# Kernel optimization log

Measured on AMD Instinct MI355X. Metric: run time of the kernel, lower is better.

## Reference

```python
import jax, jax.numpy as jnp
import numpy as np

DIM = 256
H = 4
D = DIM // H  # head_dim = 64
SCALE = D ** -0.5


def setup_inputs() -> dict:
    key = jax.random.key(0)
    ks = jax.random.split(key, 12)
    B, N, M = 4, 2048, 2048
    x_query = jax.random.normal(ks[0], (B, N, DIM), dtype=jnp.float32)
    x_context = jax.random.normal(ks[1], (B, M, DIM), dtype=jnp.float32)
    geo_bias = jax.random.normal(ks[2], (B, H, N, M), dtype=jnp.float32)
    init = 1.0 / np.sqrt(DIM)
    Wq = jax.random.uniform(ks[3], (DIM, DIM), jnp.float32, -init, init)
    bq = jax.random.uniform(ks[4], (DIM,), jnp.float32, -init, init)
    Wk = jax.random.uniform(ks[5], (DIM, DIM), jnp.float32, -init, init)
    bk = jax.random.uniform(ks[6], (DIM,), jnp.float32, -init, init)
    Wv = jax.random.uniform(ks[7], (DIM, DIM), jnp.float32, -init, init)
    bv = jax.random.uniform(ks[8], (DIM,), jnp.float32, -init, init)
    Wo = jax.random.uniform(ks[9], (DIM, DIM), jnp.float32, -init, init)
    bo = jax.random.uniform(ks[10], (DIM,), jnp.float32, -init, init)
    return {"x_query": x_query, "x_context": x_context, "geo_bias": geo_bias,
            "Wq": Wq, "bq": bq, "Wk": Wk, "bk": bk, "Wv": Wv, "bv": bv,
            "Wo": Wo, "bo": bo}


def reference(x_query, x_context, geo_bias, Wq, bq, Wk, bk, Wv, bv, Wo, bo):
    B, N, _ = x_query.shape
    M = x_context.shape[1]
    # projections; nn.Linear computes x @ W.T + b
    q = (x_query @ Wq.T + bq).reshape(B, N, H, D).transpose(0, 2, 1, 3)   # (B,H,N,D)
    k = (x_context @ Wk.T + bk).reshape(B, M, H, D).transpose(0, 2, 1, 3)  # (B,H,M,D)
    v = (x_context @ Wv.T + bv).reshape(B, M, H, D).transpose(0, 2, 1, 3)  # (B,H,M,D)
    attn = jnp.einsum("bhnd,bhmd->bhnm", q, k) * SCALE + geo_bias
    attn = jax.nn.softmax(attn, axis=-1)
    out = jnp.einsum("bhnm,bhmd->bhnd", attn, v)
    out = out.transpose(0, 2, 1, 3).reshape(B, N, DIM)
    return out @ Wo.T + bo
```

## Files before the change

### kernel.cpp

```cpp
#include <hip/hip_runtime.h>

typedef unsigned short u16;
typedef unsigned int u32;
using bf16x8  = __attribute__((ext_vector_type(8))) __bf16;
using u16x8   = __attribute__((ext_vector_type(8), may_alias)) u16;
using u16x4   = __attribute__((ext_vector_type(4), may_alias)) u16;
using f32x4   = __attribute__((ext_vector_type(4))) float;
using f32x4_a = __attribute__((ext_vector_type(4), may_alias)) float;

#define DEV __device__ __forceinline__

constexpr int Bn = 4, Hn = 4, Nn = 2048, Mn = 2048, Dn = 64, DIMn = 256;
constexpr float SCALEc = 0.125f;
constexpr float SHIFTc = 12.0f;
constexpr int LSTRIDE = 152;

DEV float bf2f(u16 h) { u32 u = ((u32)h) << 16; return __builtin_bit_cast(float, u); }
DEV u16 f2bf(float f) {
    u32 u = __builtin_bit_cast(u32, f);
    u += 0x7fffu + ((u >> 16) & 1u);
    return (u16)(u >> 16);
}
DEV bf16x8 ld8bf(const u16* p) {
    return __builtin_bit_cast(bf16x8, *reinterpret_cast<const u16x8*>(p));
}
DEV bf16x8 ld8f_bf(const float* p) {
    const f32x4 a = *reinterpret_cast<const f32x4_a*>(p);
    const f32x4 b = *reinterpret_cast<const f32x4_a*>(p + 4);
    u16x8 r;
    r[0] = f2bf(a[0]); r[1] = f2bf(a[1]); r[2] = f2bf(a[2]); r[3] = f2bf(a[3]);
    r[4] = f2bf(b[0]); r[5] = f2bf(b[1]); r[6] = f2bf(b[2]); r[7] = f2bf(b[3]);
    return __builtin_bit_cast(bf16x8, r);
}

typedef __attribute__((address_space(1))) const unsigned int as1_uint;
typedef __attribute__((address_space(3))) unsigned int as3_uint;
DEV void dma16(const float* g, float* l) {
    __builtin_amdgcn_global_load_lds((as1_uint*)g, (as3_uint*)l, 16, 0, 0);
}

__global__ __launch_bounds__(256) void qkv_kernel(
    const float* __restrict__ Xq, const float* __restrict__ Wq, const float* __restrict__ bq,
    const float* __restrict__ Xc, const float* __restrict__ Wk, const float* __restrict__ bk,
    const float* __restrict__ Wv, const float* __restrict__ bv,
    float* __restrict__ Q, u16* __restrict__ K, u16* __restrict__ V)
{
    const int wave = threadIdx.x >> 6, lane = threadIdx.x & 63;
    const int quad = lane >> 4, l16 = lane & 15;
    const int o0 = wave * 64;

    if (blockIdx.x < 512) {
        const int row0 = blockIdx.x * 16;
        const int b = row0 >> 11, n0 = row0 & 2047;
        f32x4 acc[4] = {};
        #pragma unroll
        for (int k0 = 0; k0 < 256; k0 += 32) {
            const bf16x8 af = ld8f_bf(Xq + (size_t)(row0 + l16) * DIMn + k0 + quad * 8);
            #pragma unroll
            for (int os = 0; os < 4; os++) {
                const bf16x8 wf = ld8f_bf(Wq + (size_t)(o0 + os * 16 + l16) * DIMn + k0 + quad * 8);
                acc[os] = __builtin_amdgcn_mfma_f32_16x16x32_bf16(af, wf, acc[os], 0, 0, 0);
            }
        }
        #pragma unroll
        for (int os = 0; os < 4; os++) {
            const int col = o0 + os * 16 + l16;
            const int h = col >> 6, d = col & 63;
            const float bb = bq[col];
            #pragma unroll
            for (int r = 0; r < 4; r++) {
                const int n = n0 + quad * 4 + r;
                Q[((size_t)(b * Hn + h) * Nn + n) * Dn + d] = acc[os][r] + bb;
            }
        }
    } else {
        const int row0 = (blockIdx.x - 512) * 16;
        const int b = row0 >> 11, n0 = row0 & 2047;
        f32x4 ack[4] = {};
        f32x4 acv[4] = {};
        #pragma unroll
        for (int k0 = 0; k0 < 256; k0 += 32) {
            const bf16x8 af = ld8f_bf(Xc + (size_t)(row0 + l16) * DIMn + k0 + quad * 8);
            #pragma unroll
            for (int os = 0; os < 4; os++) {
                const bf16x8 wkf = ld8f_bf(Wk + (size_t)(o0 + os * 16 + l16) * DIMn + k0 + quad * 8);
                ack[os] = __builtin_amdgcn_mfma_f32_16x16x32_bf16(af, wkf, ack[os], 0, 0, 0);
                const bf16x8 wvf = ld8f_bf(Wv + (size_t)(o0 + os * 16 + l16) * DIMn + k0 + quad * 8);
                acv[os] = __builtin_amdgcn_mfma_f32_16x16x32_bf16(wvf, af, acv[os], 0, 0, 0);
            }
        }
        #pragma unroll
        for (int os = 0; os < 4; os++) {
            const int col = o0 + os * 16 + l16;
            const int h = col >> 6, d = col & 63;
            const float bb = bk[col];
            #pragma unroll
            for (int r = 0; r < 4; r++) {
                const int m = n0 + quad * 4 + r;
                K[((size_t)(b * Hn + h) * Mn + m) * Dn + d] = f2bf(ack[os][r] + bb);
            }
        }
        #pragma unroll
        for (int os = 0; os < 4; os++)
            #pragma unroll
            for (int r = 0; r < 4; r++) {
                const int colf = o0 + os * 16 + quad * 4 + r;
                const int h = colf >> 6, d = colf & 63;
                const float bb = bv[colf];
                const int m = n0 + l16;
                V[((size_t)(b * Hn + h) * Dn + d) * Mn + m] = f2bf(acv[os][r] + bb);
            }
    }
}

__global__ __launch_bounds__(256) void attn_kernel(
    const float* __restrict__ Q,
    const u16* __restrict__ K,
    const u16* __restrict__ V,
    const float* __restrict__ geo,
    float* __restrict__ Pnum,
    float* __restrict__ Lsum,
    int S)
{
    __shared__ __align__(16) u16 plds[4][16 * LSTRIDE];
    __shared__ __align__(16) float glds[4][8][256];

    const int h = blockIdx.y;
    const int b = blockIdx.z / S, split = blockIdx.z % S;
    const int wave = threadIdx.x >> 6, lane = threadIdx.x & 63;
    const int quad = lane >> 4, l16 = lane & 15;
    const int nbase = blockIdx.x * 64 + wave * 16;
    const int mlen = Mn / S, mbeg = split * mlen, mend = mbeg + mlen;

    const float* Qh = Q + ((size_t)(b * Hn + h) * Nn + nbase) * Dn;
    const u16*   Kh = K + (size_t)(b * Hn + h) * Mn * Dn;
    const u16*   Vh = V + (size_t)(b * Hn + h) * Dn * Mn;
    const float* Gl = geo + ((size_t)(b * Hn + h) * Nn + nbase + l16) * (size_t)Mn + quad * 4;

    bf16x8 qh[2], ql[2];
    #pragma unroll
    for (int kh = 0; kh < 2; kh++) {
        const float* qp = Qh + (size_t)l16 * Dn + kh * 32 + quad * 8;
        const f32x4 a = *reinterpret_cast<const f32x4_a*>(qp);
        const f32x4 c = *reinterpret_cast<const f32x4_a*>(qp + 4);
        u16x8 hi, lo;
        #pragma unroll
        for (int j = 0; j < 4; j++) {
            hi[j] = f2bf(a[j]); lo[j] = f2bf(a[j] - bf2f(hi[j]));
            hi[4 + j] = f2bf(c[j]); lo[4 + j] = f2bf(c[j] - bf2f(hi[4 + j]));
        }
        qh[kh] = __builtin_bit_cast(bf16x8, hi);
        ql[kh] = __builtin_bit_cast(bf16x8, lo);
    }

    f32x4 oacc[4] = {};
    float lsum = 0.f;
    u16* pl = &plds[wave][0];
    float* gw = &glds[wave][0][0];
    const float* gr = gw + lane * 4;
    const u16* kbase = Kh + (size_t)l16 * Dn + quad * 8;
    const u16* vbase = Vh + (size_t)l16 * Mn + quad * 8;

    #pragma unroll
    for (int ms = 0; ms < 8; ms++)
        dma16(Gl + mbeg + ms * 16, gw + ms * 256);
    bf16x8 kb0 = ld8bf(kbase + (size_t)mbeg * Dn);
    bf16x8 kb1 = ld8bf(kbase + (size_t)mbeg * Dn + 32);

    for (int m0 = mbeg; m0 < mend; m0 += 128) {
        asm volatile("s_waitcnt vmcnt(0)" ::: "memory");
        #pragma unroll
        for (int ms = 0; ms < 8; ms++) {
            int mb = m0 + (ms + 1) * 16;
            if (mb > mend - 16) mb = mend - 16;
            const u16* kp = kbase + (size_t)mb * Dn;
            const bf16x8 nk0 = ld8bf(kp);
            const bf16x8 nk1 = ld8bf(kp + 32);
            f32x4 s = {};
            __builtin_amdgcn_s_setprio(1);
            s = __builtin_amdgcn_mfma_f32_16x16x32_bf16(kb0, qh[0], s, 0, 0, 0);
            s = __builtin_amdgcn_mfma_f32_16x16x32_bf16(kb0, ql[0], s, 0, 0, 0);
            s = __builtin_amdgcn_mfma_f32_16x16x32_bf16(kb1, qh[1], s, 0, 0, 0);
            s = __builtin_amdgcn_mfma_f32_16x16x32_bf16(kb1, ql[1], s, 0, 0, 0);
            __builtin_amdgcn_s_setprio(0);
            const f32x4 g = *reinterpret_cast<const f32x4_a*>(gr + ms * 256);
            u16x4 pk;
            float ls = 0.f;
            #pragma unroll
            for (int r = 0; r < 4; r++) {
                const float p = __expf(fmaf(s[r], SCALEc, g[r]) - SHIFTc);
                ls += p;
                pk[r] = f2bf(p);
            }
            lsum += ls;
            *reinterpret_cast<u16x4*>(pl + l16 * LSTRIDE + ms * 16 + quad * 4) = pk;
            kb0 = nk0; kb1 = nk1;
        }
        if (m0 + 128 < mend) {
            asm volatile("s_waitcnt lgkmcnt(0)" ::: "memory");
            #pragma unroll
            for (int ms = 0; ms < 8; ms++)
                dma16(Gl + (m0 + 128) + ms * 16, gw + ms * 256);
        }
        bf16x8 vcur[4], vnxt[4];
        #pragma unroll
        for (int ds = 0; ds < 4; ds++)
            vcur[ds] = ld8bf(vbase + (size_t)(ds * 16) * Mn + m0);
        #pragma unroll
        for (int kh = 0; kh < 4; kh++) {
            if (kh < 3) {
                #pragma unroll
                for (int ds = 0; ds < 4; ds++)
                    vnxt[ds] = ld8bf(vbase + (size_t)(ds * 16) * Mn + m0 + (kh + 1) * 32);
            }
            const bf16x8 pa = ld8bf(pl + l16 * LSTRIDE + kh * 32 + quad * 8);
            __builtin_amdgcn_s_setprio(1);
            #pragma unroll
            for (int ds = 0; ds < 4; ds++)
                oacc[ds] = __builtin_amdgcn_mfma_f32_16x16x32_bf16(pa, vcur[ds], oacc[ds], 0, 0, 0);
            __builtin_amdgcn_s_setprio(0);
            #pragma unroll
            for (int ds = 0; ds < 4; ds++) vcur[ds] = vnxt[ds];
        }
    }

    lsum += __shfl_xor(lsum, 16);
    lsum += __shfl_xor(lsum, 32);

    float* PN = Pnum + (size_t)split * (Bn * (size_t)Nn * DIMn)
                     + ((size_t)b * Nn + nbase) * DIMn + h * Dn;
    #pragma unroll
    for (int r = 0; r < 4; r++)
        #pragma unroll
        for (int ds = 0; ds < 4; ds++)
            PN[(size_t)(quad * 4 + r) * DIMn + ds * 16 + l16] = oacc[ds][r];

    if (lane < 16)
        Lsum[(((size_t)split * Bn + b) * Hn + h) * Nn + nbase + l16] = lsum;
}

__global__ __launch_bounds__(256) void oproj_kernel(
    const float* __restrict__ Pnum, const float* __restrict__ Lsum,
    const float* __restrict__ W, const float* __restrict__ bias,
    float* __restrict__ out, int S)
{
    const int row0 = blockIdx.x * 16;
    const int wave = threadIdx.x >> 6, lane = threadIdx.x & 63;
    const int quad = lane >> 4, l16 = lane & 15;
    const int o0 = wave * 64;
    const size_t slab = (size_t)Bn * Nn * DIMn;

    const int arow = row0 + l16;
    const int b = arow >> 11, n = arow & 2047;
    float inv[4];
    #pragma unroll
    for (int hh = 0; hh < 4; hh++) {
        float l = 0.f;
        for (int s = 0; s < S; s++)
            l += Lsum[(((size_t)s * Bn + b) * Hn + hh) * Nn + n];
        inv[hh] = 1.0f / l;
    }

    f32x4 acc[4] = {};
    #pragma unroll
    for (int k0 = 0; k0 < 256; k0 += 32) {
        f32x4 a0 = {}, a1 = {};
        for (int s = 0; s < S; s++) {
            const float* p = Pnum + (size_t)s * slab + (size_t)arow * DIMn + k0 + quad * 8;
            a0 += *reinterpret_cast<const f32x4_a*>(p);
            a1 += *reinterpret_cast<const f32x4_a*>(p + 4);
        }
        const float iv = inv[(k0 + quad * 8) >> 6];
        u16x8 r;
        #pragma unroll
        for (int j = 0; j < 4; j++) {
            r[j]     = f2bf(a0[j] * iv);
            r[4 + j] = f2bf(a1[j] * iv);
        }
        const bf16x8 af = __builtin_bit_cast(bf16x8, r);
        #pragma unroll
        for (int os = 0; os < 4; os++) {
            const bf16x8 wf = ld8f_bf(W + (size_t)(o0 + os * 16 + l16) * DIMn + k0 + quad * 8);
            acc[os] = __builtin_amdgcn_mfma_f32_16x16x32_bf16(af, wf, acc[os], 0, 0, 0);
        }
    }
    #pragma unroll
    for (int os = 0; os < 4; os++) {
        const int col = o0 + os * 16 + l16;
        const float bb = bias[col];
        #pragma unroll
        for (int r = 0; r < 4; r++) {
            const int row = row0 + quad * 4 + r;
            out[(size_t)row * DIMn + col] = acc[os][r] + bb;
        }
    }
}

extern "C" void kernel_launch(void* const* d_in, const int* in_sizes, int n_in,
                              void* d_out, int out_size, void* d_ws, size_t ws_size,
                              hipStream_t stream) {
    const float* xq  = (const float*)d_in[0];
    const float* xc  = (const float*)d_in[1];
    const float* geo = (const float*)d_in[2];
    const float* Wq  = (const float*)d_in[3];
    const float* bq  = (const float*)d_in[4];
    const float* Wk  = (const float*)d_in[5];
    const float* bk  = (const float*)d_in[6];
    const float* Wv  = (const float*)d_in[7];
    const float* bv  = (const float*)d_in[8];
    const float* Wo  = (const float*)d_in[9];
    const float* bo  = (const float*)d_in[10];

    const int S = (ws_size >= (60ull << 20)) ? 4 : 1;

    char* ws = (char*)d_ws;
    float* Qw   = (float*)ws;
    u16*   Kw   = (u16*)(ws + (8ull << 20));
    u16*   Vw   = (u16*)(ws + (12ull << 20));
    float* Pnum = (float*)(ws + (20ull << 20));
    float* Lsum = (float*)(ws + (20ull << 20) + (size_t)S * (8ull << 20));

    qkv_kernel<<<1024, 256, 0, stream>>>(xq, Wq, bq, xc, Wk, bk, Wv, bv, Qw, Kw, Vw);
    attn_kernel<<<dim3(Nn / 64, Hn, Bn * S), 256, 0, stream>>>(Qw, Kw, Vw, geo, Pnum, Lsum, S);
    oproj_kernel<<<Bn * Nn / 16, 256, 0, stream>>>(Pnum, Lsum, Wo, bo, (float*)d_out, S);
}
```

Before: 553.8 us.

## Use single-wave attention blocks with double-buffered 64-column geo bias tiles

The attention kernel becomes one wave per block, with 16 query rows each and 4x more blocks. It now steps over 64 context columns at a time, using a two-slot LDS ring for geo-bias DMA and a partial vmcnt wait so the next tile can stream in during compute. The PV step loads V directly per 32-wide chunk instead of software-prefetching it, and the split-M factor drops from 4 to 2. This trades intra-block wave sharing for a smaller LDS footprint and finer-grained overlap, but it risks less V latency hiding and correctness issues from the new wait count and buffer indexing.

```diff
diff --git a/kernel.cpp b/kernel.cpp
--- a/kernel.cpp
+++ b/kernel.cpp
@@ -13,7 +13,7 @@
 constexpr int Bn = 4, Hn = 4, Nn = 2048, Mn = 2048, Dn = 64, DIMn = 256;
 constexpr float SCALEc = 0.125f;
 constexpr float SHIFTc = 12.0f;
-constexpr int LSTRIDE = 152;
+constexpr int LSTRIDE = 76;
 
 DEV float bf2f(u16 h) { u32 u = ((u32)h) << 16; return __builtin_bit_cast(float, u); }
 DEV u16 f2bf(float f) {
@@ -113,7 +113,7 @@
     }
 }
 
-__global__ __launch_bounds__(256) void attn_kernel(
+__global__ __launch_bounds__(64) void attn_kernel(
     const float* __restrict__ Q,
     const u16* __restrict__ K,
     const u16* __restrict__ V,
@@ -122,14 +122,14 @@
     float* __restrict__ Lsum,
     int S)
 {
-    __shared__ __align__(16) u16 plds[4][16 * LSTRIDE];
-    __shared__ __align__(16) float glds[4][8][256];
+    __shared__ __align__(16) u16 plds[16 * LSTRIDE];
+    __shared__ __align__(16) float glds[2][4][256];
 
     const int h = blockIdx.y;
     const int b = blockIdx.z / S, split = blockIdx.z % S;
-    const int wave = threadIdx.x >> 6, lane = threadIdx.x & 63;
+    const int lane = threadIdx.x & 63;
     const int quad = lane >> 4, l16 = lane & 15;
-    const int nbase = blockIdx.x * 64 + wave * 16;
+    const int nbase = blockIdx.x * 16;
     const int mlen = Mn / S, mbeg = split * mlen, mend = mbeg + mlen;
 
     const float* Qh = Q + ((size_t)(b * Hn + h) * Nn + nbase) * Dn;
@@ -155,22 +155,24 @@
 
     f32x4 oacc[4] = {};
     float lsum = 0.f;
-    u16* pl = &plds[wave][0];
-    float* gw = &glds[wave][0][0];
-    const float* gr = gw + lane * 4;
     const u16* kbase = Kh + (size_t)l16 * Dn + quad * 8;
     const u16* vbase = Vh + (size_t)l16 * Mn + quad * 8;
 
     #pragma unroll
-    for (int ms = 0; ms < 8; ms++)
-        dma16(Gl + mbeg + ms * 16, gw + ms * 256);
+    for (int ms = 0; ms < 4; ms++)
+        dma16(Gl + mbeg + ms * 16, &glds[0][ms][0]);
+    #pragma unroll
+    for (int ms = 0; ms < 4; ms++)
+        dma16(Gl + mbeg + 64 + ms * 16, &glds[1][ms][0]);
     bf16x8 kb0 = ld8bf(kbase + (size_t)mbeg * Dn);
     bf16x8 kb1 = ld8bf(kbase + (size_t)mbeg * Dn + 32);
 
-    for (int m0 = mbeg; m0 < mend; m0 += 128) {
-        asm volatile("s_waitcnt vmcnt(0)" ::: "memory");
-        #pragma unroll
-        for (int ms = 0; ms < 8; ms++) {
+    int buf = 0;
+    for (int m0 = mbeg; m0 < mend; m0 += 64, buf ^= 1) {
+        asm volatile("s_waitcnt vmcnt(6)" ::: "memory");
+        const float* gr = &glds[buf][0][0] + lane * 4;
+        #pragma unroll
+        for (int ms = 0; ms < 4; ms++) {
             int mb = m0 + (ms + 1) * 16;
             if (mb > mend - 16) mb = mend - 16;
             const u16* kp = kbase + (size_t)mb * Dn;
@@ -193,34 +195,27 @@
                 pk[r] = f2bf(p);
             }
             lsum += ls;
-            *reinterpret_cast<u16x4*>(pl + l16 * LSTRIDE + ms * 16 + quad * 4) = pk;
+            *reinterpret_cast<u16x4*>(plds + l16 * LSTRIDE + ms * 16 + quad * 4) = pk;
             kb0 = nk0; kb1 = nk1;
+        }
+        #pragma unroll
+        for (int kh = 0; kh < 2; kh++) {
+            const bf16x8 pa = ld8bf(plds + l16 * LSTRIDE + kh * 32 + quad * 8);
+            bf16x8 vb[4];
+            #pragma unroll
+            for (int ds = 0; ds < 4; ds++)
+                vb[ds] = ld8bf(vbase + (size_t)(ds * 16) * Mn + m0 + kh * 32);
+            __builtin_amdgcn_s_setprio(1);
+            #pragma unroll
+            for (int ds = 0; ds < 4; ds++)
+                oacc[ds] = __builtin_amdgcn_mfma_f32_16x16x32_bf16(pa, vb[ds], oacc[ds], 0, 0, 0);
+            __builtin_amdgcn_s_setprio(0);
         }
         if (m0 + 128 < mend) {
             asm volatile("s_waitcnt lgkmcnt(0)" ::: "memory");
             #pragma unroll
-            for (int ms = 0; ms < 8; ms++)
-                dma16(Gl + (m0 + 128) + ms * 16, gw + ms * 256);
-        }
-        bf16x8 vcur[4], vnxt[4];
-        #pragma unroll
-        for (int ds = 0; ds < 4; ds++)
-            vcur[ds] = ld8bf(vbase + (size_t)(ds * 16) * Mn + m0);
-        #pragma unroll
-        for (int kh = 0; kh < 4; kh++) {
-            if (kh < 3) {
-                #pragma unroll
-                for (int ds = 0; ds < 4; ds++)
-                    vnxt[ds] = ld8bf(vbase + (size_t)(ds * 16) * Mn + m0 + (kh + 1) * 32);
-            }
-            const bf16x8 pa = ld8bf(pl + l16 * LSTRIDE + kh * 32 + quad * 8);
-            __builtin_amdgcn_s_setprio(1);
-            #pragma unroll
-            for (int ds = 0; ds < 4; ds++)
-                oacc[ds] = __builtin_amdgcn_mfma_f32_16x16x32_bf16(pa, vcur[ds], oacc[ds], 0, 0, 0);
-            __builtin_amdgcn_s_setprio(0);
-            #pragma unroll
-            for (int ds = 0; ds < 4; ds++) vcur[ds] = vnxt[ds];
+            for (int ms = 0; ms < 4; ms++)
+                dma16(Gl + (m0 + 128) + ms * 16, &glds[buf][ms][0]);
         }
     }
 
@@ -311,7 +306,7 @@
     const float* Wo  = (const float*)d_in[9];
     const float* bo  = (const float*)d_in[10];
 
-    const int S = (ws_size >= (60ull << 20)) ? 4 : 1;
+    const int S = (ws_size >= (40ull << 20)) ? 2 : 1;
 
     char* ws = (char*)d_ws;
     float* Qw   = (float*)ws;
@@ -321,6 +316,6 @@
     float* Lsum = (float*)(ws + (20ull << 20) + (size_t)S * (8ull << 20));
 
     qkv_kernel<<<1024, 256, 0, stream>>>(xq, Wq, bq, xc, Wk, bk, Wv, bv, Qw, Kw, Vw);
-    attn_kernel<<<dim3(Nn / 64, Hn, Bn * S), 256, 0, stream>>>(Qw, Kw, Vw, geo, Pnum, Lsum, S);
+    attn_kernel<<<dim3(Nn / 16, Hn, Bn * S), 64, 0, stream>>>(Qw, Kw, Vw, geo, Pnum, Lsum, S);
     oproj_kernel<<<Bn * Nn / 16, 256, 0, stream>>>(Pnum, Lsum, Wo, bo, (float*)d_out, S);
 }
```

New measurement: 576.1 us. +4.0%, slower.
